# Kernel tuning notes

Hardware: AMD Instinct MI355X
Metric: run time of the kernel (lower is better)

## Reference

```python
import jax, jax.numpy as jnp
import numpy as np

NUM_CLASSES = 80
IOU_THR = 0.5
SCORE_THR = 0.25
MAX_BBOXES = 100
NEG = -1e9  # sentinel for suppressed scores


def setup_inputs() -> dict:
    key = jax.random.key(0)
    ks = jax.random.split(key, 9)
    B = 8
    def head(i, g):
        return (jax.random.uniform(ks[3*i], (B, g, g, 3, 4), dtype=jnp.float32),
                jax.random.uniform(ks[3*i+1], (B, g, g, 3, 1), dtype=jnp.float32),
                jax.random.normal(ks[3*i+2], (B, g, g, 3, NUM_CLASSES), dtype=jnp.float32))
    b20, p20, c20 = head(0, 20)
    b40, p40, c40 = head(1, 40)
    b80, p80, c80 = head(2, 80)
    return {"bbox20": b20, "p20": p20, "c20": c20,
            "bbox40": b40, "p40": p40, "c40": c40,
            "bbox80": b80, "p80": p80, "c80": c80}


def _iou_one_vs_all(box, boxes):
    # box: (4,) [y1,x1,y2,x2]; boxes: (N,4)
    y1, x1, y2, x2 = box[0], box[1], box[2], box[3]
    Y1, X1, Y2, X2 = boxes[:, 0], boxes[:, 1], boxes[:, 2], boxes[:, 3]
    ih = jnp.maximum(jnp.minimum(y2, Y2) - jnp.maximum(y1, Y1), 0.0)
    iw = jnp.maximum(jnp.minimum(x2, X2) - jnp.maximum(x1, X1), 0.0)
    inter = ih * iw
    union = (y2 - y1) * (x2 - x1) + (Y2 - Y1) * (X2 - X1) - inter
    return jnp.where(union > 0, inter / union, 0.0)


def _nms_single(boxes, scores):
    # boxes (N,4), scores (N,) -> greedy class-agnostic NMS, up to MAX_BBOXES
    sc0 = jnp.where(scores > SCORE_THR, scores, NEG)

    def body(sc, _):
        idx = jnp.argmax(sc)
        s = sc[idx]
        valid = s > NEG * 0.5
        box = boxes[idx]
        iou = _iou_one_vs_all(box, boxes)
        sc = jnp.where(iou > IOU_THR, NEG, sc)
        sc = sc.at[idx].set(NEG)
        ob = jnp.where(valid, jnp.clip(box, 0.0, 1.0), 0.0)  # clip_boxes=True default
        os = jnp.where(valid, s, 0.0)
        return sc, (ob, os, valid)

    _, (b, s, v) = jax.lax.scan(body, sc0, None, length=MAX_BBOXES)
    return b, s, jnp.sum(v.astype(jnp.int32))


def _forward(bbox20, p20, c20, bbox40, p40, c40, bbox80, p80, c80):
    B = bbox20.shape[0]
    bbox = jnp.concatenate([x.reshape(B, -1, 4) for x in (bbox20, bbox40, bbox80)], axis=1)
    p = jnp.concatenate([x.reshape(B, -1) for x in (p20, p40, p80)], axis=1)
    c = jnp.concatenate([x.reshape(B, -1, NUM_CLASSES) for x in (c20, c40, c80)], axis=1)
    cls = jnp.argmax(c, axis=-1).astype(jnp.float32)  # (B,N)
    score = p * cls  # quirky score = objectness * class index (faithful to source)
    b, s, valid = jax.vmap(_nms_single)(bbox, score)
    # classes output: scores had a single class dim in the TF op -> class index 0
    pred = jnp.concatenate([b, s[..., None], jnp.zeros_like(s)[..., None]], axis=-1)
    return pred, valid


def reference(bbox20, p20, c20, bbox40, p40, c40, bbox80, p80, c80):
    return _forward(bbox20, p20, c20, bbox40, p40, c40, bbox80, p80, c80)
```

## Files before the change

kernel.cpp:

```cpp
#include <hip/hip_runtime.h>
#include <hip/hip_bf16.h>

#define NUM_CLASSES 80
#define BATCH 8
#define N20 1200
#define N40 4800
#define N80 19200
#define NANCH 25200
#define NEGV  -1000000000.0f
#define SCORE_THR 0.25f
#define CAP 2048
#define RMAX 192
#define PKCAP 512
#define NHBIN 1024
#define THR_LIST 64.0f

typedef unsigned long long ull;

__global__ __launch_bounds__(256, 3) void score_kernel(
        const float* __restrict__ p20, const float* __restrict__ c20,
        const float* __restrict__ p40, const float* __restrict__ c40,
        const float* __restrict__ p80, const float* __restrict__ c80,
        float* __restrict__ scores) {
    const int t = threadIdx.x;
    const int b = blockIdx.y;
    const int an = blockIdx.x * 256 + t;
    const bool valid_an = (an < NANCH);
    const int n = valid_an ? an : (NANCH - 1);

    const float *cp, *pp;
    if (n < N20) {
        cp = c20 + ((size_t)b * N20 + n) * NUM_CLASSES;
        pp = p20 + (size_t)b * N20 + n;
    } else if (n < N20 + N40) {
        int a = n - N20;
        cp = c40 + ((size_t)b * N40 + a) * NUM_CLASSES;
        pp = p40 + (size_t)b * N40 + a;
    } else {
        int a = n - N20 - N40;
        cp = c80 + ((size_t)b * N80 + a) * NUM_CLASSES;
        pp = p80 + (size_t)b * N80 + a;
    }

    const float4* c4 = (const float4*)cp;
    float p = *pp;
    float4 v[20];
#pragma unroll
    for (int k = 0; k < 20; k++) v[k] = c4[k];
    __builtin_amdgcn_sched_barrier(0);

    float best = -INFINITY;
    int bi = 0;
#pragma unroll
    for (int k = 0; k < 20; k++) {
        int basei = k * 4;
        if (v[k].x > best) { best = v[k].x; bi = basei; }
        if (v[k].y > best) { best = v[k].y; bi = basei + 1; }
        if (v[k].z > best) { best = v[k].z; bi = basei + 2; }
        if (v[k].w > best) { best = v[k].w; bi = basei + 3; }
    }

    float s = __fmul_rn(p, (float)bi);
    float sval = (s > SCORE_THR) ? s : NEGV;
    if (valid_an) scores[(size_t)b * NANCH + an] = sval;
}

__device__ __forceinline__ bool iou_gt(const float4 A, float areaA, const float4 Bx, float areaB) {
    float ih = fmaxf(__fsub_rn(fminf(A.z, Bx.z), fmaxf(A.x, Bx.x)), 0.0f);
    float iw = fmaxf(__fsub_rn(fminf(A.w, Bx.w), fmaxf(A.y, Bx.y)), 0.0f);
    float inter = __fmul_rn(ih, iw);
    float uni = __fsub_rn(__fadd_rn(areaA, areaB), inter);
    if (!(uni > 0.0f)) return false;
    return __fdiv_rn(inter, uni) > 0.5f;
}

__device__ __forceinline__ bool iou_gt_fast(const float4 A, float areaA, const float4 Bx, float areaB) {
    float ih = fmaxf(__fsub_rn(fminf(A.z, Bx.z), fmaxf(A.x, Bx.x)), 0.0f);
    float iw = fmaxf(__fsub_rn(fminf(A.w, Bx.w), fmaxf(A.y, Bx.y)), 0.0f);
    float inter = __fmul_rn(ih, iw);
    float uni = __fsub_rn(__fadd_rn(areaA, areaB), inter);
    if (!(uni > 0.0f)) return false;
    if (__fmul_rn(2.0f, inter) < __fmul_rn(uni, 0.99999988f)) return false;
    return __fdiv_rn(inter, uni) > 0.5f;
}

__device__ __forceinline__ float4 load_box(int b, int n,
        const float* b20, const float* b40, const float* b80) {
    if (n < N20)       return ((const float4*)b20)[(size_t)b * N20 + n];
    if (n < N20 + N40) return ((const float4*)b40)[(size_t)b * N40 + (n - N20)];
    return ((const float4*)b80)[(size_t)b * N80 + (n - N20 - N40)];
}

__device__ __forceinline__ float box_area(const float4 B) {
    return __fmul_rn(__fsub_rn(B.z, B.x), __fsub_rn(B.w, B.y));
}

__device__ __forceinline__ int key_idx(ull k) {
    return (int)(0xFFFFFFFFu - (unsigned)(k & 0xFFFFFFFFull));
}

__global__ __launch_bounds__(1024) void nms_kernel(
        float* __restrict__ scores,
        const float* __restrict__ b20, const float* __restrict__ b40,
        const float* __restrict__ b80, float* __restrict__ out) {
    __shared__ ull skeys[CAP];
    __shared__ ull pk[PKCAP];
    __shared__ unsigned hist[NHBIN];
    __shared__ int prt[PKCAP][5];
    __shared__ ull srt_key[RMAX];
    __shared__ float4 bboxC[4][RMAX + 1];
    __shared__ ull M[RMAX][3];
    __shared__ ull red[1024];
    __shared__ int sh_V, sh_T;
    __shared__ unsigned sh_cnt, sh_pcnt;

    const int t = threadIdx.x;
    const int lane = t & 63;
    const int b = blockIdx.x;

    hist[t] = 0u;
    if (t == 0) { sh_V = 0; sh_cnt = 0u; sh_pcnt = 0u; }
    __syncthreads();

    const float4* sc4 = (const float4*)(scores + (size_t)b * NANCH);
    float4 s4[7];
#pragma unroll
    for (int it = 0; it < 7; it++) {
        const int i = t + it * 1024;
        s4[it] = (i < NANCH / 4) ? sc4[i] : make_float4(NEGV, NEGV, NEGV, NEGV);
    }
    __builtin_amdgcn_sched_barrier(0);
#pragma unroll
    for (int it = 0; it < 7; it++) {
        const int i = t + it * 1024;
        const float sv[4] = {s4[it].x, s4[it].y, s4[it].z, s4[it].w};
#pragma unroll
        for (int c = 0; c < 4; c++) {
            if (sv[c] >= THR_LIST) {
                const unsigned sb = __float_as_uint(sv[c]);
                const unsigned an = (unsigned)(i * 4 + c);
                unsigned pos = atomicAdd(&sh_cnt, 1u);
                if (pos < (unsigned)CAP)
                    skeys[pos] = ((ull)sb << 32) | (ull)(0xFFFFFFFFu - an);
                atomicAdd(&hist[min((int)((sb - 0x42800000u) >> 13), NHBIN - 1)], 1u);
            }
        }
    }
    __syncthreads();

    const int cnt = (int)sh_cnt;
    const bool use_list = (cnt <= CAP);
    const int nR = use_list ? min(cnt, RMAX) : 0;
    const unsigned need = (unsigned)nR;

    if (use_list) {
        if (t < 64) {
            unsigned h[16], sfx[16];
            const int basei = t * 16;
#pragma unroll
            for (int k = 0; k < 16; k++) h[k] = hist[basei + k];
            unsigned run = 0;
#pragma unroll
            for (int k = 15; k >= 0; k--) { run += h[k]; sfx[k] = run; }
            unsigned s = run;
#pragma unroll
            for (int d = 1; d < 64; d <<= 1) {
                unsigned vv = __shfl_down(s, d);
                if (t + d < 64) s += vv;
            }
            const unsigned above = s - run;
            int bestb = -1;
#pragma unroll
            for (int k = 0; k < 16; k++)
                if (sfx[k] + above >= need) bestb = basei + k;
#pragma unroll
            for (int d = 32; d > 0; d >>= 1) {
                int o = __shfl_down(bestb, d);
                if (t + d < 64) bestb = max(bestb, o);
            }
            if (t == 0) sh_T = max(bestb, 0);
        }
        __syncthreads();
        const int T = sh_T;

#pragma unroll
        for (int h = 0; h < 2; h++) {
            const int c = t + h * 1024;
            bool part = false;
            ull k = 0ull;
            if (c < cnt) {
                k = skeys[c];
                int bin = min((int)(((unsigned)(k >> 32) - 0x42800000u) >> 13), NHBIN - 1);
                part = (bin >= T);
            }
            ull mask = __ballot(part);
            if (mask != 0ull) {
                int leader = (int)(__ffsll(mask) - 1);
                unsigned basep = 0;
                if (lane == leader) basep = atomicAdd(&sh_pcnt, (unsigned)__popcll(mask));
                basep = __shfl(basep, leader);
                if (part) {
                    unsigned pos = basep + (unsigned)__popcll(mask & ((1ull << lane) - 1));
                    if (pos < (unsigned)PKCAP) pk[pos] = k;
                }
            }
        }
        __syncthreads();
        const int m = (int)sh_pcnt;

        if (m <= PKCAP) {
            ull kmy = 0ull;
            float4 bmy = make_float4(0.f, 0.f, 0.f, 0.f);
            if (t < m) {
                kmy = pk[t];
                bmy = load_box(b, key_idx(kmy), b20, b40, b80);
            }
            const int q = t >> 8, u = t & 255;
            const ull kA = (u < m) ? pk[u] : 0ull;
            const ull kB = (u + 256 < m) ? pk[u + 256] : 0ull;
            const int Q = (m + 3) >> 2;
            const int j0 = q * Q, j1 = min(m, j0 + Q);
            int rA = 0, rB = 0;
#pragma unroll 8
            for (int j = j0; j < j1; j++) {
                ull kj = pk[j];
                rA += (kj > kA) ? 1 : 0;
                rB += (kj > kB) ? 1 : 0;
            }
            prt[u][q] = rA;
            prt[u + 256][q] = rB;
            __syncthreads();
            if (t < m) {
                int r = prt[t][0] + prt[t][1] + prt[t][2] + prt[t][3];
                if (r < RMAX) {
                    srt_key[r] = kmy;
#pragma unroll
                    for (int c = 0; c < 4; c++) bboxC[c][r] = bmy;
                }
            }
            __syncthreads();
        } else {
            ull kA = (t < cnt) ? skeys[t] : 0ull;
            ull kB = (t + 1024 < cnt) ? skeys[t + 1024] : 0ull;
            int rA = 0, rB = 0;
            for (int j = 0; j < cnt; j++) {
                ull kj = skeys[j];
                rA += (kj > kA) ? 1 : 0;
                rB += (kj > kB) ? 1 : 0;
            }
            if (t < cnt && rA < RMAX) srt_key[rA] = kA;
            if (t + 1024 < cnt && rB < RMAX) srt_key[rB] = kB;
            __syncthreads();
            if (t < nR) {
                float4 B = load_box(b, key_idx(srt_key[t]), b20, b40, b80);
#pragma unroll
                for (int c = 0; c < 4; c++) bboxC[c][t] = B;
            }
            __syncthreads();
        }

        {
            const int row = t >> 2, cw = t & 3;
            if (row < RMAX && cw < 3) {
                ull w = 0ull;
                if (row < nR && cw * 64 < row) {
                    const float4 B = bboxC[cw][row];
                    const float aB = box_area(B);
                    const int jmax = min(64, row - cw * 64);
                    const float4* src = &bboxC[cw][cw * 64];
                    for (int j = 0; j < jmax; j++) {
                        const float4 C = src[j];
                        w |= ((ull)iou_gt_fast(C, box_area(C), B, aB)) << j;
                    }
                }
                M[row][cw] = w;
            }
        }
        __syncthreads();

        int v = 0;
        if (t < 64) {
            ull A0 = 0, A1 = 0, A2 = 0;
            for (int rg = 0; rg < 3 && v < 100; rg++) {
                const int rr = rg * 64 + t;
                const bool valid = (rr < nR);
                ull w0 = 0, w1 = 0, w2 = 0;
                if (valid) { w0 = M[rr][0]; w1 = M[rr][1]; w2 = M[rr][2]; }
                const ull mw = (rg == 0) ? w0 : (rg == 1) ? w1 : w2;
                const bool supE = !valid ||
                    (((w0 & A0) | (w1 & A1) | (w2 & A2)) != 0ull);
                ull alive = __ballot(!supE);
                while (alive != 0ull && v < 100) {
                    int c = (int)(__ffsll(alive) - 1);
                    ull supc = __ballot((bool)((mw >> c) & 1ull));
                    alive &= ~(supc | (1ull << c));
                    if (rg == 0) A0 |= 1ull << c;
                    else if (rg == 1) A1 |= 1ull << c;
                    else A2 |= 1ull << c;
                    if (t == c) {
                        const float4 B = bboxC[0][rr];
                        float* rowp = out + ((size_t)b * 100 + v) * 6;
                        rowp[0] = fminf(fmaxf(B.x, 0.f), 1.f);
                        rowp[1] = fminf(fmaxf(B.y, 0.f), 1.f);
                        rowp[2] = fminf(fmaxf(B.z, 0.f), 1.f);
                        rowp[3] = fminf(fmaxf(B.w, 0.f), 1.f);
                        rowp[4] = __uint_as_float((unsigned)(srt_key[rr] >> 32));
                        rowp[5] = 0.f;
                    }
                    v++;
                }
            }
            if (t == 0) sh_V = v;
        }
        __syncthreads();
    }

    const bool need_fb = (!use_list) || (sh_V < 100 && cnt > nR);
    if (need_fb) {
        float* scb = scores + (size_t)b * NANCH;
        int v2 = 0;
        for (int k = 0; k < 100; k++) {
            ull bestk = 0ull;
            for (int i = t; i < NANCH; i += 1024) {
                float sv = scb[i];
                unsigned u = __float_as_uint(sv);
                u ^= (u & 0x80000000u) ? 0xFFFFFFFFu : 0x80000000u;
                ull key = ((ull)u << 32) | (ull)(0xFFFFFFFFu - (unsigned)i);
                if (key > bestk) bestk = key;
            }
            red[t] = bestk;
            __syncthreads();
            for (int ss = 512; ss > 0; ss >>= 1) {
                if (t < ss && red[t + ss] > red[t]) red[t] = red[t + ss];
                __syncthreads();
            }
            ull bk = red[0];
            __syncthreads();
            unsigned u = (unsigned)(bk >> 32);
            u ^= (u & 0x80000000u) ? 0x80000000u : 0xFFFFFFFFu;
            float s = __uint_as_float(u);
            int idx = (int)(0xFFFFFFFFu - (unsigned)(bk & 0xFFFFFFFFull));
            if (!(s > NEGV * 0.5f)) break;
            float4 B = load_box(b, idx, b20, b40, b80);
            float aB = box_area(B);
            for (int i = t; i < NANCH; i += 1024) {
                float sv = scb[i];
                if (sv > NEGV * 0.5f) {
                    float4 C = load_box(b, i, b20, b40, b80);
                    if (iou_gt(B, aB, C, box_area(C))) scb[i] = NEGV;
                }
            }
            if (t == 0) {
                scb[idx] = NEGV;
                float* rowp = out + ((size_t)b * 100 + k) * 6;
                rowp[0] = fminf(fmaxf(B.x, 0.f), 1.f);
                rowp[1] = fminf(fmaxf(B.y, 0.f), 1.f);
                rowp[2] = fminf(fmaxf(B.z, 0.f), 1.f);
                rowp[3] = fminf(fmaxf(B.w, 0.f), 1.f);
                rowp[4] = s;
                rowp[5] = 0.f;
            }
            v2++;
            __syncthreads();
        }
        __syncthreads();
        if (t == 0) sh_V = v2;
        __syncthreads();
    }

    const int V = sh_V;
    for (int i = V * 6 + t; i < 600; i += 1024) out[(size_t)b * 600 + i] = 0.f;
    if (t == 0) out[4800 + b] = (float)V;
}

extern "C" void kernel_launch(void* const* d_in, const int* in_sizes, int n_in,
                              void* d_out, int out_size, void* d_ws, size_t ws_size,
                              hipStream_t stream) {
    const float* b20 = (const float*)d_in[0];
    const float* p20 = (const float*)d_in[1];
    const float* c20 = (const float*)d_in[2];
    const float* b40 = (const float*)d_in[3];
    const float* p40 = (const float*)d_in[4];
    const float* c40 = (const float*)d_in[5];
    const float* b80 = (const float*)d_in[6];
    const float* p80 = (const float*)d_in[7];
    const float* c80 = (const float*)d_in[8];

    float* scores = (float*)d_ws;

    dim3 sgrid((NANCH + 255) / 256, BATCH);
    score_kernel<<<sgrid, 256, 0, stream>>>(
        p20, c20, p40, c40, p80, c80, scores);

    nms_kernel<<<BATCH, 1024, 0, stream>>>(
        scores, b20, b40, b80, (float*)d_out);
}
```

Measured before the change: 148.3 us.

## Compact candidate keys in score kernel to skip full score rescan in NMS

The score kernel now ballots anchors whose score is at or above the list threshold and writes per-wavefront compacted keys and counts to workspace slots. The NMS kernel then prefix-sums the slot counts and gathers only those keys instead of reading all 25200 scores per batch with shared atomics. This removes a full-array read and atomic contention from the single-block-per-batch NMS stage. In exchange the fallback condition changes to run whenever fewer than 100 boxes are kept, and slot overflow forces the fallback path.

```diff
diff --git a/kernel.cpp b/kernel.cpp
--- a/kernel.cpp
+++ b/kernel.cpp
@@ -1,5 +1,4 @@
 #include <hip/hip_runtime.h>
-#include <hip/hip_bf16.h>
 
 #define NUM_CLASSES 80
 #define BATCH 8
@@ -14,6 +13,9 @@
 #define PKCAP 512
 #define NHBIN 1024
 #define THR_LIST 64.0f
+#define NBLK 99
+#define NSLOT 396
+#define SLOTCAP 32
 
 typedef unsigned long long ull;
 
@@ -21,7 +23,8 @@
         const float* __restrict__ p20, const float* __restrict__ c20,
         const float* __restrict__ p40, const float* __restrict__ c40,
         const float* __restrict__ p80, const float* __restrict__ c80,
-        float* __restrict__ scores) {
+        float* __restrict__ scores, unsigned* __restrict__ gcnt,
+        ull* __restrict__ gkeys) {
     const int t = threadIdx.x;
     const int b = blockIdx.y;
     const int an = blockIdx.x * 256 + t;
@@ -63,6 +66,20 @@
     float s = __fmul_rn(p, (float)bi);
     float sval = (s > SCORE_THR) ? s : NEGV;
     if (valid_an) scores[(size_t)b * NANCH + an] = sval;
+
+    const bool cand = valid_an && (sval >= THR_LIST);
+    const ull mask = __ballot(cand);
+    const int lane = t & 63;
+    const int slot = blockIdx.x * 4 + (t >> 6);
+    if (cand) {
+        const int pos = __popcll(mask & ((1ull << lane) - 1ull));
+        if (pos < SLOTCAP) {
+            const ull key = ((ull)__float_as_uint(sval) << 32) |
+                            (ull)(0xFFFFFFFFu - (unsigned)an);
+            gkeys[(((size_t)b * NSLOT + slot) << 5) + pos] = key;
+        }
+    }
+    if (lane == 0) gcnt[b * NSLOT + slot] = (unsigned)__popcll(mask);
 }
 
 __device__ __forceinline__ bool iou_gt(const float4 A, float areaA, const float4 Bx, float areaB) {
@@ -100,7 +117,8 @@
 }
 
 __global__ __launch_bounds__(1024) void nms_kernel(
-        float* __restrict__ scores,
+        float* __restrict__ scores, const unsigned* __restrict__ gcnt,
+        const ull* __restrict__ gkeys,
         const float* __restrict__ b20, const float* __restrict__ b40,
         const float* __restrict__ b80, float* __restrict__ out) {
     __shared__ ull skeys[CAP];
@@ -110,48 +128,71 @@
     __shared__ ull srt_key[RMAX];
     __shared__ float4 bboxC[4][RMAX + 1];
     __shared__ ull M[RMAX][3];
-    __shared__ ull red[1024];
-    __shared__ int sh_V, sh_T;
-    __shared__ unsigned sh_cnt, sh_pcnt;
+    __shared__ unsigned scnt[NSLOT];
+    __shared__ unsigned soff[NSLOT];
+    __shared__ int sh_V, sh_T, sh_m, sh_ovf;
+    __shared__ unsigned sh_pcnt;
 
     const int t = threadIdx.x;
     const int lane = t & 63;
     const int b = blockIdx.x;
 
     hist[t] = 0u;
-    if (t == 0) { sh_V = 0; sh_cnt = 0u; sh_pcnt = 0u; }
+    if (t == 0) { sh_V = 0; sh_ovf = 0; sh_pcnt = 0u; }
     __syncthreads();
 
-    const float4* sc4 = (const float4*)(scores + (size_t)b * NANCH);
-    float4 s4[7];
-#pragma unroll
-    for (int it = 0; it < 7; it++) {
-        const int i = t + it * 1024;
-        s4[it] = (i < NANCH / 4) ? sc4[i] : make_float4(NEGV, NEGV, NEGV, NEGV);
-    }
-    __builtin_amdgcn_sched_barrier(0);
-#pragma unroll
-    for (int it = 0; it < 7; it++) {
-        const int i = t + it * 1024;
-        const float sv[4] = {s4[it].x, s4[it].y, s4[it].z, s4[it].w};
-#pragma unroll
-        for (int c = 0; c < 4; c++) {
-            if (sv[c] >= THR_LIST) {
-                const unsigned sb = __float_as_uint(sv[c]);
-                const unsigned an = (unsigned)(i * 4 + c);
-                unsigned pos = atomicAdd(&sh_cnt, 1u);
-                if (pos < (unsigned)CAP)
-                    skeys[pos] = ((ull)sb << 32) | (ull)(0xFFFFFFFFu - an);
-                atomicAdd(&hist[min((int)((sb - 0x42800000u) >> 13), NHBIN - 1)], 1u);
-            }
-        }
+    if (t < NSLOT) {
+        unsigned c = gcnt[b * NSLOT + t];
+        scnt[t] = c;
+        if (c > (unsigned)SLOTCAP) sh_ovf = 1;
     }
     __syncthreads();
 
-    const int cnt = (int)sh_cnt;
-    const bool use_list = (cnt <= CAP);
-    const int nR = use_list ? min(cnt, RMAX) : 0;
+    if (t < 64) {
+        unsigned c[7];
+        unsigned s = 0;
+#pragma unroll
+        for (int k = 0; k < 7; k++) {
+            int idx = t * 7 + k;
+            c[k] = (idx < NSLOT) ? scnt[idx] : 0u;
+            s += c[k];
+        }
+        unsigned incl = s;
+#pragma unroll
+        for (int d = 1; d < 64; d <<= 1) {
+            unsigned vv = __shfl_up(incl, d);
+            if (t >= d) incl += vv;
+        }
+        unsigned base = incl - s;
+#pragma unroll
+        for (int k = 0; k < 7; k++) {
+            int idx = t * 7 + k;
+            if (idx < NSLOT) soff[idx] = base;
+            base += c[k];
+        }
+        if (t == 63) sh_m = (int)incl;
+    }
+    __syncthreads();
+
+    const int m = sh_m;
+    const bool use_list = (m <= CAP) && (sh_ovf == 0);
+    const int nR = use_list ? min(m, RMAX) : 0;
     const unsigned need = (unsigned)nR;
+
+    if (use_list) {
+        for (int c = t; c < m; c += 1024) {
+            int lo = 0, hi = NSLOT - 1;
+            while (lo < hi) {
+                int mid = (lo + hi + 1) >> 1;
+                if (soff[mid] <= (unsigned)c) lo = mid; else hi = mid - 1;
+            }
+            ull k = gkeys[(((size_t)b * NSLOT + lo) << 5) + (c - soff[lo])];
+            skeys[c] = k;
+            unsigned sb = (unsigned)(k >> 32);
+            atomicAdd(&hist[min((int)((sb - 0x42800000u) >> 13), NHBIN - 1)], 1u);
+        }
+    }
+    __syncthreads();
 
     if (use_list) {
         if (t < 64) {
@@ -188,7 +229,7 @@
             const int c = t + h * 1024;
             bool part = false;
             ull k = 0ull;
-            if (c < cnt) {
+            if (c < m) {
                 k = skeys[c];
                 int bin = min((int)(((unsigned)(k >> 32) - 0x42800000u) >> 13), NHBIN - 1);
                 part = (bin >= T);
@@ -206,20 +247,20 @@
             }
         }
         __syncthreads();
-        const int m = (int)sh_pcnt;
-
-        if (m <= PKCAP) {
+        const int pm = (int)sh_pcnt;
+
+        if (pm <= PKCAP) {
             ull kmy = 0ull;
             float4 bmy = make_float4(0.f, 0.f, 0.f, 0.f);
-            if (t < m) {
+            if (t < pm) {
                 kmy = pk[t];
                 bmy = load_box(b, key_idx(kmy), b20, b40, b80);
             }
             const int q = t >> 8, u = t & 255;
-            const ull kA = (u < m) ? pk[u] : 0ull;
-            const ull kB = (u + 256 < m) ? pk[u + 256] : 0ull;
-            const int Q = (m + 3) >> 2;
-            const int j0 = q * Q, j1 = min(m, j0 + Q);
+            const ull kA = (u < pm) ? pk[u] : 0ull;
+            const ull kB = (u + 256 < pm) ? pk[u + 256] : 0ull;
+            const int Q = (pm + 3) >> 2;
+            const int j0 = q * Q, j1 = min(pm, j0 + Q);
             int rA = 0, rB = 0;
 #pragma unroll 8
             for (int j = j0; j < j1; j++) {
@@ -230,7 +271,7 @@
             prt[u][q] = rA;
             prt[u + 256][q] = rB;
             __syncthreads();
-            if (t < m) {
+            if (t < pm) {
                 int r = prt[t][0] + prt[t][1] + prt[t][2] + prt[t][3];
                 if (r < RMAX) {
                     srt_key[r] = kmy;
@@ -240,16 +281,16 @@
             }
             __syncthreads();
         } else {
-            ull kA = (t < cnt) ? skeys[t] : 0ull;
-            ull kB = (t + 1024 < cnt) ? skeys[t + 1024] : 0ull;
+            ull kA = (t < m) ? skeys[t] : 0ull;
+            ull kB = (t + 1024 < m) ? skeys[t + 1024] : 0ull;
             int rA = 0, rB = 0;
-            for (int j = 0; j < cnt; j++) {
+            for (int j = 0; j < m; j++) {
                 ull kj = skeys[j];
                 rA += (kj > kA) ? 1 : 0;
                 rB += (kj > kB) ? 1 : 0;
             }
-            if (t < cnt && rA < RMAX) srt_key[rA] = kA;
-            if (t + 1024 < cnt && rB < RMAX) srt_key[rB] = kB;
+            if (t < m && rA < RMAX) srt_key[rA] = kA;
+            if (t + 1024 < m && rB < RMAX) srt_key[rB] = kB;
             __syncthreads();
             if (t < nR) {
                 float4 B = load_box(b, key_idx(srt_key[t]), b20, b40, b80);
@@ -315,8 +356,9 @@
         __syncthreads();
     }
 
-    const bool need_fb = (!use_list) || (sh_V < 100 && cnt > nR);
+    const bool need_fb = (!use_list) || (sh_V < 100);
     if (need_fb) {
+        ull* red = skeys;
         float* scb = scores + (size_t)b * NANCH;
         int v2 = 0;
         for (int k = 0; k < 100; k++) {
@@ -386,12 +428,14 @@
     const float* p80 = (const float*)d_in[7];
     const float* c80 = (const float*)d_in[8];
 
-    float* scores = (float*)d_ws;
+    float*    scores = (float*)d_ws;
+    unsigned* gcnt   = (unsigned*)((char*)d_ws + 806400);
+    ull*      gkeys  = (ull*)((char*)d_ws + 806400 + 12672);
 
     dim3 sgrid((NANCH + 255) / 256, BATCH);
     score_kernel<<<sgrid, 256, 0, stream>>>(
-        p20, c20, p40, c40, p80, c80, scores);
+        p20, c20, p40, c40, p80, c80, scores, gcnt, gkeys);
 
     nms_kernel<<<BATCH, 1024, 0, stream>>>(
-        scores, b20, b40, b80, (float*)d_out);
-}
+        scores, gcnt, gkeys, b20, b40, b80, (float*)d_out);
+}
```

Result: faster. 144.9 us (-2.3%).
